# Performance work log

Hardware: AMD Instinct MI355X
Metric: run time of the kernel (lower is better)

## Reference

```python
import jax, jax.numpy as jnp
import numpy as np

HID = 128          # hidden_dim
NF = 8             # n_features of reconstructed PathFeatureExtractor
S0 = 100.0
T = 1.0
XI0 = 0.235 ** 2
ETA_REF = 1.9
DELTA_IDX = 3      # PathFeatureExtractor.DELTA_PREV_INDEX
NEG_SLOPE = 0.2


def _features(S):
    """Causal per-step path features. S: (B, n+1) -> (B, n, NF)."""
    B, np1 = S.shape
    n = np1 - 1
    logm = jnp.log(S / S0)                       # (B, n+1) log-moneyness
    x = logm[:, :n]                              # value at step k
    ret = jnp.diff(logm, axis=1)                 # (B, n) log returns
    qv_full = jnp.cumsum(ret ** 2, axis=1)
    qv = jnp.concatenate([jnp.zeros((B, 1), S.dtype), qv_full[:, :-1]], axis=1)  # QV up to step k
    k = jnp.arange(n, dtype=S.dtype)
    t = k / n * T
    tau = (T - t) / T                            # normalized time to maturity
    run_mean = jnp.cumsum(x, axis=1) / (k + 1.0)
    ones = jnp.ones_like(x)
    feats = jnp.stack([
        x,                                       # 0: log(S_k/S0)
        tau * ones,                              # 1: time to maturity
        jnp.sqrt(XI0) * ones,                    # 2: ref vol
        jnp.zeros_like(x),                       # 3: delta_prev slot (injected in scan)
        run_mean,                                # 4: running mean log-price (sig level 1)
        qv,                                      # 5: realized quadratic variation (sig level 2 diag)
        ETA_REF * jnp.sqrt(qv + 1e-12),          # 6: vol-of-vol scaled QV
        (t / T) * ones,                          # 7: elapsed time
    ], axis=-1)
    return feats


def _mlp(feat, W0, b0, rW1, rb1, rW2, rb2, sW1, sb1, sW2, sb2, Wf, bf):
    lrelu = lambda v: jax.nn.leaky_relu(v, NEG_SLOPE)
    h = lrelu(feat @ W0 + b0)
    h = h + (lrelu(h @ rW1 + rb1) @ rW2 + rb2)   # ResidualBlock 1
    h = h + (lrelu(h @ sW1 + sb1) @ sW2 + sb2)   # ResidualBlock 2
    return jax.nn.sigmoid(h @ Wf + bf)[:, 0]


def _linear_params(key, fan_in, fan_out):
    kw, kb = jax.random.split(key)
    bound = 1.0 / np.sqrt(fan_in)
    W = jax.random.uniform(kw, (fan_in, fan_out), jnp.float32, -bound, bound)
    b = jax.random.uniform(kb, (fan_out,), jnp.float32, -bound, bound)
    return W, b


def setup_inputs() -> dict:
    key = jax.random.key(0)
    ks = jax.random.split(key, 6)
    B, n = 32768, 64
    # GBM-like price paths starting at S0
    incr = 0.02 * jax.random.normal(ks[0], (B, n), jnp.float32)
    logpath = jnp.concatenate([jnp.zeros((B, 1), jnp.float32), jnp.cumsum(incr, axis=1)], axis=1)
    S = S0 * jnp.exp(logpath)
    W0, b0 = _linear_params(ks[1], NF, HID)
    rW1, rb1 = _linear_params(ks[2], HID, HID)
    rW2, rb2 = _linear_params(jax.random.fold_in(ks[2], 1), HID, HID)
    sW1, sb1 = _linear_params(ks[3], HID, HID)
    sW2, sb2 = _linear_params(jax.random.fold_in(ks[3], 1), HID, HID)
    Wf, bf = _linear_params(ks[4], HID, 1)
    return {"S": S, "W0": W0, "b0": b0, "rW1": rW1, "rb1": rb1, "rW2": rW2, "rb2": rb2,
            "sW1": sW1, "sb1": sb1, "sW2": sW2, "sb2": sb2, "Wf": Wf, "bf": bf}


def reference(S, W0, b0, rW1, rb1, rW2, rb2, sW1, sb1, sW2, sb2, Wf, bf):
    feats = _features(S).astype(jnp.float32)          # (B, n, NF)
    fT = jnp.transpose(feats, (1, 0, 2))              # (n, B, NF) for scan
    B = S.shape[0]

    def step(delta_prev, feat_k):
        # inject detached delta_{k-1} at feature index 3 (matches .detach())
        feat_k = feat_k.at[:, DELTA_IDX].set(jax.lax.stop_gradient(delta_prev))
        d = _mlp(feat_k, W0, b0, rW1, rb1, rW2, rb2, sW1, sb1, sW2, sb2, Wf, bf)
        return d, d

    _, deltas = jax.lax.scan(step, jnp.zeros((B,), jnp.float32), fT)
    return jnp.transpose(deltas)                      # (B, n)
```

## Files before the change

### kernel.cpp

```cpp
#include <hip/hip_runtime.h>
#include <math.h>

#define HID 128
#define NSTEPS 64
#define SLEN 65
#define THREADS 256
#define ROWS 64
#define ASTRIDE 136
#define FSTRIDE 40
#define DSTR 68

typedef _Float16 half8 __attribute__((ext_vector_type(8)));
typedef __fp16 fp16x2 __attribute__((ext_vector_type(2)));
typedef float floatx4 __attribute__((ext_vector_type(4)));

__global__ __launch_bounds__(THREADS, 2)
void hedger(const float* __restrict__ S,
            const float* __restrict__ W0,  const float* __restrict__ b0,
            const float* __restrict__ rW1, const float* __restrict__ rb1,
            const float* __restrict__ rW2, const float* __restrict__ rb2,
            const float* __restrict__ sW1, const float* __restrict__ sb1,
            const float* __restrict__ sW2, const float* __restrict__ sb2,
            const float* __restrict__ Wf,  const float* __restrict__ bfp,
            float* __restrict__ out)
{
  __shared__ __align__(16) _Float16 bufA[ROWS * ASTRIDE];
  __shared__ __align__(16) _Float16 bufB[ROWS * ASTRIDE];
  __shared__ __align__(16) _Float16 featb[ROWS * FSTRIDE];
  __shared__ __align__(16) _Float16 WfS[HID];
  __shared__ __align__(16) float    Slds[ROWS * SLEN];
  __shared__ __align__(16) float    deltab[ROWS * DSTR];

  const int tid  = threadIdx.x;
  const int wave = tid >> 6;
  const int lane = tid & 63;
  const int l15  = lane & 15;
  const int quad = lane >> 4;
  const int n_base = wave * 32;
  const int r0 = blockIdx.x * ROWS;
  const int col0 = n_base + 2 * l15;

  half8 wfrag[4][4][2];
  {
    const float* Wm[4] = {rW1, rW2, sW1, sW2};
#pragma unroll
    for (int m = 0; m < 4; ++m)
#pragma unroll
      for (int kq = 0; kq < 4; ++kq)
#pragma unroll
        for (int nt = 0; nt < 2; ++nt) {
          const int n  = col0 + nt;
          const int kb = kq * 32 + quad * 8;
          half8 f;
#pragma unroll
          for (int j = 0; j < 8; ++j)
            f[j] = (_Float16)Wm[m][(kb + j) * HID + n];
          wfrag[m][kq][nt] = f;
        }
  }
  half8 w0frag[2];
#pragma unroll
  for (int nt = 0; nt < 2; ++nt) {
    const int n = col0 + nt;
    half8 f;
#pragma unroll
    for (int j = 0; j < 8; ++j) {
      const int k = quad * 8 + j;
      f[j] = (k < 8) ? (_Float16)W0[k * HID + n] : (_Float16)0.f;
    }
    w0frag[nt] = f;
  }
  float b0r[2], rb1r[2], rb2r[2], sb1r[2], sb2r[2];
#pragma unroll
  for (int nt = 0; nt < 2; ++nt) {
    const int n = col0 + nt;
    b0r[nt] = b0[n]; rb1r[nt] = rb1[n]; rb2r[nt] = rb2[n];
    sb1r[nt] = sb1[n]; sb2r[nt] = sb2[n];
  }
  const float bfv = bfp[0];

  for (int i = tid; i < ROWS * FSTRIDE; i += THREADS) featb[i] = (_Float16)0.f;
  if (tid < HID) WfS[tid] = (_Float16)Wf[tid];
  for (int i = tid; i < ROWS * SLEN; i += THREADS)
    Slds[i] = S[(size_t)r0 * SLEN + i];
  __syncthreads();

  float lm_prev = 0.f, cum_x = 0.f, qv = 0.f;
  const float* Srow = &Slds[(tid & (ROWS - 1)) * SLEN];
  if (tid < ROWS) {
    const float lm = logf(Srow[0] * 0.01f);
    lm_prev = lm; cum_x = lm; qv = 0.f;
    _Float16* fr = &featb[tid * FSTRIDE];
    fr[0] = (_Float16)lm;
    fr[1] = (_Float16)1.0f;
    fr[2] = (_Float16)0.235f;
    fr[3] = (_Float16)0.f;
    fr[4] = (_Float16)lm;
    fr[5] = (_Float16)0.f;
    fr[6] = (_Float16)(1.9f * sqrtf(1e-12f));
    fr[7] = (_Float16)0.f;
  }
  __syncthreads();

  floatx4 acc[4][2];

#define INIT_BIAS(BR) do { \
  _Pragma("unroll") for (int mt = 0; mt < 4; ++mt) \
  _Pragma("unroll") for (int nt = 0; nt < 2; ++nt) { \
    floatx4 z = {BR[nt], BR[nt], BR[nt], BR[nt]}; acc[mt][nt] = z; } } while (0)

#define INIT_BIAS_RES(BR, RESBUF) do { \
  _Pragma("unroll") for (int mt = 0; mt < 4; ++mt) \
  _Pragma("unroll") for (int r = 0; r < 4; ++r) { \
    const int row = mt * 16 + quad * 4 + r; \
    const fp16x2 h2 = *(const fp16x2*)&RESBUF[row * ASTRIDE + col0]; \
    acc[mt][0][r] = BR[0] + (float)h2[0]; \
    acc[mt][1][r] = BR[1] + (float)h2[1]; \
  } } while (0)

#define GEMM128(SRC, MI) do { \
  _Pragma("unroll") for (int kq = 0; kq < 4; ++kq) { \
    half8 afr[4]; \
    _Pragma("unroll") for (int mt = 0; mt < 4; ++mt) \
      afr[mt] = *(const half8*)&SRC[(mt * 16 + l15) * ASTRIDE + kq * 32 + quad * 8]; \
    _Pragma("unroll") for (int mt = 0; mt < 4; ++mt) \
    _Pragma("unroll") for (int nt = 0; nt < 2; ++nt) \
      acc[mt][nt] = __builtin_amdgcn_mfma_f32_16x16x32_f16( \
          afr[mt], wfrag[MI][kq][nt], acc[mt][nt], 0, 0, 0); \
  } } while (0)

#define EPI_LRELU(DST) do { \
  _Pragma("unroll") for (int mt = 0; mt < 4; ++mt) \
  _Pragma("unroll") for (int r = 0; r < 4; ++r) { \
    const int row = mt * 16 + quad * 4 + r; \
    const float v0 = acc[mt][0][r]; \
    const float v1 = acc[mt][1][r]; \
    fp16x2 h2 = {(__fp16)fmaxf(v0, 0.2f * v0), (__fp16)fmaxf(v1, 0.2f * v1)}; \
    *(fp16x2*)&DST[row * ASTRIDE + col0] = h2; \
  } } while (0)

#define EPI_STORE(DST) do { \
  _Pragma("unroll") for (int mt = 0; mt < 4; ++mt) \
  _Pragma("unroll") for (int r = 0; r < 4; ++r) { \
    const int row = mt * 16 + quad * 4 + r; \
    fp16x2 h2 = {(__fp16)acc[mt][0][r], (__fp16)acc[mt][1][r]}; \
    *(fp16x2*)&DST[row * ASTRIDE + col0] = h2; \
  } } while (0)

#pragma unroll 1
  for (int k = 0; k < NSTEPS; ++k) {
    INIT_BIAS(b0r);
    {
      half8 afr[4];
#pragma unroll
      for (int mt = 0; mt < 4; ++mt)
        afr[mt] = *(const half8*)&featb[(mt * 16 + l15) * FSTRIDE + quad * 8];
#pragma unroll
      for (int mt = 0; mt < 4; ++mt)
#pragma unroll
        for (int nt = 0; nt < 2; ++nt)
          acc[mt][nt] = __builtin_amdgcn_mfma_f32_16x16x32_f16(
              afr[mt], w0frag[nt], acc[mt][nt], 0, 0, 0);
    }
    EPI_LRELU(bufA);
    __syncthreads();

    if (tid < ROWS) {
      const int kk = k + 1;
      const float lm = logf(Srow[kk] * 0.01f);
      const float rr = lm - lm_prev; qv += rr * rr;
      lm_prev = lm; cum_x += lm;
      const float tT = (float)kk * (1.f / 64.f);
      _Float16* fr = &featb[tid * FSTRIDE];
      fr[0] = (_Float16)lm;
      fr[1] = (_Float16)(1.f - tT);
      fr[4] = (_Float16)(cum_x / (float)(kk + 1));
      fr[5] = (_Float16)qv;
      fr[6] = (_Float16)(1.9f * sqrtf(qv + 1e-12f));
      fr[7] = (_Float16)tT;
    }

    INIT_BIAS(rb1r);            GEMM128(bufA, 0); EPI_LRELU(bufB);
    __syncthreads();
    INIT_BIAS_RES(rb2r, bufA);  GEMM128(bufB, 1); EPI_STORE(bufA);
    __syncthreads();
    INIT_BIAS(sb1r);            GEMM128(bufA, 2); EPI_LRELU(bufB);
    __syncthreads();
    INIT_BIAS_RES(sb2r, bufA);  GEMM128(bufB, 3); EPI_STORE(bufA);
    __syncthreads();

    {
      floatx4 dacc = {0.f, 0.f, 0.f, 0.f};
#pragma unroll
      for (int kq = 0; kq < 4; ++kq) {
        const half8 a  = *(const half8*)&bufA[(wave * 16 + l15) * ASTRIDE + kq * 32 + quad * 8];
        const half8 wv = *(const half8*)&WfS[kq * 32 + quad * 8];
        dacc = __builtin_amdgcn_mfma_f32_16x16x32_f16(a, wv, dacc, 0, 0, 0);
      }
      if (l15 < 4) {
        const float sv = (l15 & 2) ? ((l15 & 1) ? dacc[3] : dacc[2])
                                   : ((l15 & 1) ? dacc[1] : dacc[0]);
        const int row = wave * 16 + quad * 4 + l15;
        const float d = 1.f / (1.f + expf(-(sv + bfv)));
        featb[row * FSTRIDE + 3] = (_Float16)d;
        deltab[row * DSTR + k] = d;
      }
    }
    __syncthreads();
  }

  {
    const int row = tid >> 2;
    const int c0  = (tid & 3) * 16;
    const float* dr = &deltab[row * DSTR + c0];
    float* orow = &out[(size_t)(r0 + row) * NSTEPS + c0];
#pragma unroll
    for (int u = 0; u < 4; ++u) {
      const floatx4 v = *(const floatx4*)&dr[u * 4];
      *(floatx4*)&orow[u * 4] = v;
    }
  }
#undef INIT_BIAS
#undef INIT_BIAS_RES
#undef GEMM128
#undef EPI_LRELU
#undef EPI_STORE
}

extern "C" void kernel_launch(void* const* d_in, const int* in_sizes, int n_in,
                              void* d_out, int out_size, void* d_ws, size_t ws_size,
                              hipStream_t stream) {
  const float* S   = (const float*)d_in[0];
  const float* W0  = (const float*)d_in[1];
  const float* b0  = (const float*)d_in[2];
  const float* rW1 = (const float*)d_in[3];
  const float* rb1 = (const float*)d_in[4];
  const float* rW2 = (const float*)d_in[5];
  const float* rb2 = (const float*)d_in[6];
  const float* sW1 = (const float*)d_in[7];
  const float* sb1 = (const float*)d_in[8];
  const float* sW2 = (const float*)d_in[9];
  const float* sb2 = (const float*)d_in[10];
  const float* Wf  = (const float*)d_in[11];
  const float* bf  = (const float*)d_in[12];
  float* out = (float*)d_out;

  const int B = out_size / NSTEPS;
  const int nblocks = B / ROWS;
  hedger<<<nblocks, THREADS, 0, stream>>>(
      S, W0, b0, rW1, rb1, rW2, rb2, sW1, sb1, sW2, sb2, Wf, bf, out);
}
```

Baseline: 395.4 us.

## Double threads per block so each wave owns 16 output columns

Raises the block to 512 threads (8 waves), so each wave computes a 16-column slice instead of 32. That halves the per-thread weight-fragment registers and accumulators, and W0 and the biases move to LDS to save further registers. The aim is more waves per CU to hide MFMA and LDS latency in this sync-heavy sequential scan. In exchange the epilogue stores become scalar fp16 writes, barriers span twice as many waves, and the bias and W0 fragments are now reloaded from LDS every step.

```diff
diff --git a/kernel.cpp b/kernel.cpp
--- a/kernel.cpp
+++ b/kernel.cpp
@@ -4,7 +4,7 @@
 #define HID 128
 #define NSTEPS 64
 #define SLEN 65
-#define THREADS 256
+#define THREADS 512
 #define ROWS 64
 #define ASTRIDE 136
 #define FSTRIDE 40
@@ -14,7 +14,7 @@
 typedef __fp16 fp16x2 __attribute__((ext_vector_type(2)));
 typedef float floatx4 __attribute__((ext_vector_type(4)));
 
-__global__ __launch_bounds__(THREADS, 2)
+__global__ __launch_bounds__(THREADS, 4)
 void hedger(const float* __restrict__ S,
             const float* __restrict__ W0,  const float* __restrict__ b0,
             const float* __restrict__ rW1, const float* __restrict__ rb1,
@@ -28,6 +28,8 @@
   __shared__ __align__(16) _Float16 bufB[ROWS * ASTRIDE];
   __shared__ __align__(16) _Float16 featb[ROWS * FSTRIDE];
   __shared__ __align__(16) _Float16 WfS[HID];
+  __shared__ __align__(16) _Float16 W0B[HID * 8];
+  __shared__ __align__(16) float    biasL[5 * HID];
   __shared__ __align__(16) float    Slds[ROWS * SLEN];
   __shared__ __align__(16) float    deltab[ROWS * DSTR];
 
@@ -36,51 +38,37 @@
   const int lane = tid & 63;
   const int l15  = lane & 15;
   const int quad = lane >> 4;
-  const int n_base = wave * 32;
-  const int r0 = blockIdx.x * ROWS;
-  const int col0 = n_base + 2 * l15;
-
-  half8 wfrag[4][4][2];
+  const int col  = wave * 16 + l15;
+  const int r0   = blockIdx.x * ROWS;
+
+  half8 wfrag[4][4];
   {
     const float* Wm[4] = {rW1, rW2, sW1, sW2};
 #pragma unroll
     for (int m = 0; m < 4; ++m)
 #pragma unroll
-      for (int kq = 0; kq < 4; ++kq)
-#pragma unroll
-        for (int nt = 0; nt < 2; ++nt) {
-          const int n  = col0 + nt;
-          const int kb = kq * 32 + quad * 8;
-          half8 f;
-#pragma unroll
-          for (int j = 0; j < 8; ++j)
-            f[j] = (_Float16)Wm[m][(kb + j) * HID + n];
-          wfrag[m][kq][nt] = f;
-        }
-  }
-  half8 w0frag[2];
-#pragma unroll
-  for (int nt = 0; nt < 2; ++nt) {
-    const int n = col0 + nt;
-    half8 f;
-#pragma unroll
-    for (int j = 0; j < 8; ++j) {
-      const int k = quad * 8 + j;
-      f[j] = (k < 8) ? (_Float16)W0[k * HID + n] : (_Float16)0.f;
-    }
-    w0frag[nt] = f;
-  }
-  float b0r[2], rb1r[2], rb2r[2], sb1r[2], sb2r[2];
-#pragma unroll
-  for (int nt = 0; nt < 2; ++nt) {
-    const int n = col0 + nt;
-    b0r[nt] = b0[n]; rb1r[nt] = rb1[n]; rb2r[nt] = rb2[n];
-    sb1r[nt] = sb1[n]; sb2r[nt] = sb2[n];
+      for (int kq = 0; kq < 4; ++kq) {
+        const int kb = kq * 32 + quad * 8;
+        half8 f;
+#pragma unroll
+        for (int j = 0; j < 8; ++j)
+          f[j] = (_Float16)Wm[m][(kb + j) * HID + col];
+        wfrag[m][kq] = f;
+      }
   }
   const float bfv = bfp[0];
 
   for (int i = tid; i < ROWS * FSTRIDE; i += THREADS) featb[i] = (_Float16)0.f;
-  if (tid < HID) WfS[tid] = (_Float16)Wf[tid];
+  if (tid < HID) {
+    WfS[tid] = (_Float16)Wf[tid];
+#pragma unroll
+    for (int j = 0; j < 8; ++j) W0B[tid * 8 + j] = (_Float16)W0[j * HID + tid];
+    biasL[0 * HID + tid] = b0[tid];
+    biasL[1 * HID + tid] = rb1[tid];
+    biasL[2 * HID + tid] = rb2[tid];
+    biasL[3 * HID + tid] = sb1[tid];
+    biasL[4 * HID + tid] = sb2[tid];
+  }
   for (int i = tid; i < ROWS * SLEN; i += THREADS)
     Slds[i] = S[(size_t)r0 * SLEN + i];
   __syncthreads();
@@ -102,20 +90,19 @@
   }
   __syncthreads();
 
-  floatx4 acc[4][2];
-
-#define INIT_BIAS(BR) do { \
-  _Pragma("unroll") for (int mt = 0; mt < 4; ++mt) \
-  _Pragma("unroll") for (int nt = 0; nt < 2; ++nt) { \
-    floatx4 z = {BR[nt], BR[nt], BR[nt], BR[nt]}; acc[mt][nt] = z; } } while (0)
-
-#define INIT_BIAS_RES(BR, RESBUF) do { \
+  floatx4 acc[4];
+
+#define INIT_BIAS(BI) do { \
+  const float bv = biasL[(BI) * HID + col]; \
+  _Pragma("unroll") for (int mt = 0; mt < 4; ++mt) { \
+    floatx4 z = {bv, bv, bv, bv}; acc[mt] = z; } } while (0)
+
+#define INIT_BIAS_RES(BI, RESBUF) do { \
+  const float bv = biasL[(BI) * HID + col]; \
   _Pragma("unroll") for (int mt = 0; mt < 4; ++mt) \
   _Pragma("unroll") for (int r = 0; r < 4; ++r) { \
     const int row = mt * 16 + quad * 4 + r; \
-    const fp16x2 h2 = *(const fp16x2*)&RESBUF[row * ASTRIDE + col0]; \
-    acc[mt][0][r] = BR[0] + (float)h2[0]; \
-    acc[mt][1][r] = BR[1] + (float)h2[1]; \
+    acc[mt][r] = bv + (float)RESBUF[row * ASTRIDE + col]; \
   } } while (0)
 
 #define GEMM128(SRC, MI) do { \
@@ -124,43 +111,40 @@
     _Pragma("unroll") for (int mt = 0; mt < 4; ++mt) \
       afr[mt] = *(const half8*)&SRC[(mt * 16 + l15) * ASTRIDE + kq * 32 + quad * 8]; \
     _Pragma("unroll") for (int mt = 0; mt < 4; ++mt) \
-    _Pragma("unroll") for (int nt = 0; nt < 2; ++nt) \
-      acc[mt][nt] = __builtin_amdgcn_mfma_f32_16x16x32_f16( \
-          afr[mt], wfrag[MI][kq][nt], acc[mt][nt], 0, 0, 0); \
+      acc[mt] = __builtin_amdgcn_mfma_f32_16x16x32_f16( \
+          afr[mt], wfrag[MI][kq], acc[mt], 0, 0, 0); \
   } } while (0)
 
 #define EPI_LRELU(DST) do { \
   _Pragma("unroll") for (int mt = 0; mt < 4; ++mt) \
   _Pragma("unroll") for (int r = 0; r < 4; ++r) { \
     const int row = mt * 16 + quad * 4 + r; \
-    const float v0 = acc[mt][0][r]; \
-    const float v1 = acc[mt][1][r]; \
-    fp16x2 h2 = {(__fp16)fmaxf(v0, 0.2f * v0), (__fp16)fmaxf(v1, 0.2f * v1)}; \
-    *(fp16x2*)&DST[row * ASTRIDE + col0] = h2; \
+    const float v0 = acc[mt][r]; \
+    DST[row * ASTRIDE + col] = (_Float16)fmaxf(v0, 0.2f * v0); \
   } } while (0)
 
 #define EPI_STORE(DST) do { \
   _Pragma("unroll") for (int mt = 0; mt < 4; ++mt) \
   _Pragma("unroll") for (int r = 0; r < 4; ++r) { \
     const int row = mt * 16 + quad * 4 + r; \
-    fp16x2 h2 = {(__fp16)acc[mt][0][r], (__fp16)acc[mt][1][r]}; \
-    *(fp16x2*)&DST[row * ASTRIDE + col0] = h2; \
+    DST[row * ASTRIDE + col] = (_Float16)acc[mt][r]; \
   } } while (0)
 
 #pragma unroll 1
   for (int k = 0; k < NSTEPS; ++k) {
-    INIT_BIAS(b0r);
+    INIT_BIAS(0);
     {
+      half8 w0f;
+      if (quad == 0) w0f = *(const half8*)&W0B[col * 8];
+      else { half8 z = {0,0,0,0,0,0,0,0}; w0f = z; }
       half8 afr[4];
 #pragma unroll
       for (int mt = 0; mt < 4; ++mt)
         afr[mt] = *(const half8*)&featb[(mt * 16 + l15) * FSTRIDE + quad * 8];
 #pragma unroll
       for (int mt = 0; mt < 4; ++mt)
-#pragma unroll
-        for (int nt = 0; nt < 2; ++nt)
-          acc[mt][nt] = __builtin_amdgcn_mfma_f32_16x16x32_f16(
-              afr[mt], w0frag[nt], acc[mt][nt], 0, 0, 0);
+        acc[mt] = __builtin_amdgcn_mfma_f32_16x16x32_f16(
+            afr[mt], w0f, acc[mt], 0, 0, 0);
     }
     EPI_LRELU(bufA);
     __syncthreads();
@@ -180,16 +164,16 @@
       fr[7] = (_Float16)tT;
     }
 
-    INIT_BIAS(rb1r);            GEMM128(bufA, 0); EPI_LRELU(bufB);
-    __syncthreads();
-    INIT_BIAS_RES(rb2r, bufA);  GEMM128(bufB, 1); EPI_STORE(bufA);
-    __syncthreads();
-    INIT_BIAS(sb1r);            GEMM128(bufA, 2); EPI_LRELU(bufB);
-    __syncthreads();
-    INIT_BIAS_RES(sb2r, bufA);  GEMM128(bufB, 3); EPI_STORE(bufA);
-    __syncthreads();
-
-    {
+    INIT_BIAS(1);               GEMM128(bufA, 0); EPI_LRELU(bufB);
+    __syncthreads();
+    INIT_BIAS_RES(2, bufA);     GEMM128(bufB, 1); EPI_STORE(bufA);
+    __syncthreads();
+    INIT_BIAS(3);               GEMM128(bufA, 2); EPI_LRELU(bufB);
+    __syncthreads();
+    INIT_BIAS_RES(4, bufA);     GEMM128(bufB, 3); EPI_STORE(bufA);
+    __syncthreads();
+
+    if (wave < 4) {
       floatx4 dacc = {0.f, 0.f, 0.f, 0.f};
 #pragma unroll
       for (int kq = 0; kq < 4; ++kq) {
@@ -210,12 +194,12 @@
   }
 
   {
-    const int row = tid >> 2;
-    const int c0  = (tid & 3) * 16;
+    const int row = tid >> 3;
+    const int c0  = (tid & 7) * 8;
     const float* dr = &deltab[row * DSTR + c0];
     float* orow = &out[(size_t)(r0 + row) * NSTEPS + c0];
 #pragma unroll
-    for (int u = 0; u < 4; ++u) {
+    for (int u = 0; u < 2; ++u) {
       const floatx4 v = *(const floatx4*)&dr[u * 4];
       *(floatx4*)&orow[u * 4] = v;
     }
```

Measured after the change: 550.7 us. 1.39x slower.

## Fold last residual linear layer into final projection vector

Applied to the files above, without the earlier changes.

Because the last residual block's second linear layer feeds straight into the linear output head, the kernel precomputes sW2·Wf and sb2·Wf+bf once per block. The final 128x128 GEMM and one barrier per step are replaced by an extra dot-product MFMA on bufB. This removes a quarter of the per-step GEMM work and frees the registers that held one weight fragment set. In exchange, each block redundantly does a serial 128-term dot product per thread at setup, and the fp16 rounding of the fused vector slightly changes numerics.

```diff
diff --git a/kernel.cpp b/kernel.cpp
--- a/kernel.cpp
+++ b/kernel.cpp
@@ -28,6 +28,8 @@
   __shared__ __align__(16) _Float16 bufB[ROWS * ASTRIDE];
   __shared__ __align__(16) _Float16 featb[ROWS * FSTRIDE];
   __shared__ __align__(16) _Float16 WfS[HID];
+  __shared__ __align__(16) _Float16 Ws2S[HID];
+  __shared__             float    CvalS;
   __shared__ __align__(16) float    Slds[ROWS * SLEN];
   __shared__ __align__(16) float    deltab[ROWS * DSTR];
 
@@ -40,11 +42,11 @@
   const int r0 = blockIdx.x * ROWS;
   const int col0 = n_base + 2 * l15;
 
-  half8 wfrag[4][4][2];
+  half8 wfrag[3][4][2];
   {
-    const float* Wm[4] = {rW1, rW2, sW1, sW2};
-#pragma unroll
-    for (int m = 0; m < 4; ++m)
+    const float* Wm[3] = {rW1, rW2, sW1};
+#pragma unroll
+    for (int m = 0; m < 3; ++m)
 #pragma unroll
       for (int kq = 0; kq < 4; ++kq)
 #pragma unroll
@@ -70,20 +72,30 @@
     }
     w0frag[nt] = f;
   }
-  float b0r[2], rb1r[2], rb2r[2], sb1r[2], sb2r[2];
+  float b0r[2], rb1r[2], rb2r[2], sb1r[2];
 #pragma unroll
   for (int nt = 0; nt < 2; ++nt) {
     const int n = col0 + nt;
-    b0r[nt] = b0[n]; rb1r[nt] = rb1[n]; rb2r[nt] = rb2[n];
-    sb1r[nt] = sb1[n]; sb2r[nt] = sb2[n];
-  }
-  const float bfv = bfp[0];
+    b0r[nt] = b0[n]; rb1r[nt] = rb1[n]; rb2r[nt] = rb2[n]; sb1r[nt] = sb1[n];
+  }
 
   for (int i = tid; i < ROWS * FSTRIDE; i += THREADS) featb[i] = (_Float16)0.f;
-  if (tid < HID) WfS[tid] = (_Float16)Wf[tid];
+  if (tid < HID) {
+    WfS[tid] = (_Float16)Wf[tid];
+    float s = 0.f;
+    for (int n = 0; n < HID; ++n) s += sW2[tid * HID + n] * Wf[n];
+    Ws2S[tid] = (_Float16)s;
+  }
+  if (wave == 0) {
+    float p = sb2[lane] * Wf[lane] + sb2[lane + 64] * Wf[lane + 64];
+    p += __shfl_xor(p, 1);  p += __shfl_xor(p, 2);  p += __shfl_xor(p, 4);
+    p += __shfl_xor(p, 8);  p += __shfl_xor(p, 16); p += __shfl_xor(p, 32);
+    if (lane == 0) CvalS = p + bfp[0];
+  }
   for (int i = tid; i < ROWS * SLEN; i += THREADS)
     Slds[i] = S[(size_t)r0 * SLEN + i];
   __syncthreads();
+  const float Cval = CvalS;
 
   float lm_prev = 0.f, cum_x = 0.f, qv = 0.f;
   const float* Srow = &Slds[(tid & (ROWS - 1)) * SLEN];
@@ -186,22 +198,27 @@
     __syncthreads();
     INIT_BIAS(sb1r);            GEMM128(bufA, 2); EPI_LRELU(bufB);
     __syncthreads();
-    INIT_BIAS_RES(sb2r, bufA);  GEMM128(bufB, 3); EPI_STORE(bufA);
-    __syncthreads();
 
     {
-      floatx4 dacc = {0.f, 0.f, 0.f, 0.f};
+      floatx4 dacc  = {0.f, 0.f, 0.f, 0.f};
+      floatx4 dacc2 = {0.f, 0.f, 0.f, 0.f};
 #pragma unroll
       for (int kq = 0; kq < 4; ++kq) {
-        const half8 a  = *(const half8*)&bufA[(wave * 16 + l15) * ASTRIDE + kq * 32 + quad * 8];
-        const half8 wv = *(const half8*)&WfS[kq * 32 + quad * 8];
-        dacc = __builtin_amdgcn_mfma_f32_16x16x32_f16(a, wv, dacc, 0, 0, 0);
+        const int off = kq * 32 + quad * 8;
+        const half8 a1 = *(const half8*)&bufA[(wave * 16 + l15) * ASTRIDE + off];
+        const half8 w1 = *(const half8*)&WfS[off];
+        dacc  = __builtin_amdgcn_mfma_f32_16x16x32_f16(a1, w1, dacc, 0, 0, 0);
+        const half8 a2 = *(const half8*)&bufB[(wave * 16 + l15) * ASTRIDE + off];
+        const half8 w2 = *(const half8*)&Ws2S[off];
+        dacc2 = __builtin_amdgcn_mfma_f32_16x16x32_f16(a2, w2, dacc2, 0, 0, 0);
       }
       if (l15 < 4) {
-        const float sv = (l15 & 2) ? ((l15 & 1) ? dacc[3] : dacc[2])
+        const float s1 = (l15 & 2) ? ((l15 & 1) ? dacc[3] : dacc[2])
                                    : ((l15 & 1) ? dacc[1] : dacc[0]);
+        const float s2 = (l15 & 2) ? ((l15 & 1) ? dacc2[3] : dacc2[2])
+                                   : ((l15 & 1) ? dacc2[1] : dacc2[0]);
         const int row = wave * 16 + quad * 4 + l15;
-        const float d = 1.f / (1.f + expf(-(sv + bfv)));
+        const float d = 1.f / (1.f + expf(-(s1 + s2 + Cval)));
         featb[row * FSTRIDE + 3] = (_Float16)d;
         deltab[row * DSTR + k] = d;
       }
```

After: 345.6 us. 12.6% less time.
